# Optimization experiments

Hardware: AMD Instinct MI355X
Metric: run time of the kernel (lower is better)

Reference implementation:

```python
import jax, jax.numpy as jnp
import numpy as np

NUM_GRAPHS = 1024  # static number of segments for global_mean_pool


def setup_inputs() -> dict:
    key = jax.random.key(0)
    ks = jax.random.split(key, 16)
    N, E, F_IN, H = 100000, 1000000, 32, 64
    NUM_ATOM, NUM_ACT, L = 16, 8, 3
    s = 0.05
    x = jax.random.normal(ks[0], (N, F_IN), dtype=jnp.float32)
    edge_index = jax.random.randint(ks[1], (2, E), 0, N, dtype=jnp.int64)
    batch = jnp.sort(jax.random.randint(ks[2], (N,), 0, NUM_GRAPHS, dtype=jnp.int64))
    W_emb = jax.random.normal(ks[3], (F_IN, H), dtype=jnp.float32) * s
    b_emb = jnp.zeros((H,), dtype=jnp.float32)
    W_convs = jax.random.normal(ks[4], (L, H, H), dtype=jnp.float32) * s
    b_convs = jnp.zeros((L, H), dtype=jnp.float32)
    W_act = jax.random.normal(ks[5], (H, NUM_ACT), dtype=jnp.float32) * s
    b_act = jnp.zeros((NUM_ACT,), dtype=jnp.float32)
    W_tgt = jax.random.normal(ks[6], (H, 1), dtype=jnp.float32) * s
    b_tgt = jnp.zeros((1,), dtype=jnp.float32)
    W_atom = jax.random.normal(ks[7], (H, NUM_ATOM), dtype=jnp.float32) * s
    b_atom = jnp.zeros((NUM_ATOM,), dtype=jnp.float32)
    return {"x": x, "edge_index": edge_index, "batch": batch,
            "W_emb": W_emb, "b_emb": b_emb, "W_convs": W_convs, "b_convs": b_convs,
            "W_act": W_act, "b_act": b_act, "W_tgt": W_tgt, "b_tgt": b_tgt,
            "W_atom": W_atom, "b_atom": b_atom}


def reference(x, edge_index, batch, W_emb, b_emb, W_convs, b_convs,
              W_act, b_act, W_tgt, b_tgt, W_atom, b_atom):
    N = x.shape[0]
    # --- GCN normalization with self-loops (PyG GCNConv default) ---
    self_idx = jnp.arange(N, dtype=edge_index.dtype)
    src = jnp.concatenate([edge_index[0], self_idx])  # message source (row)
    dst = jnp.concatenate([edge_index[1], self_idx])  # aggregation target (col)
    ones_e = jnp.ones(src.shape[0], dtype=x.dtype)
    deg = jax.ops.segment_sum(ones_e, dst, num_segments=N)  # in-degree + self-loop
    dinv = jnp.where(deg > 0, jax.lax.rsqrt(deg), 0.0)
    norm = (dinv[src] * dinv[dst])[:, None]  # [E+N, 1]

    h = jax.nn.relu(x @ W_emb + b_emb)  # node embedding
    for i in range(W_convs.shape[0]):
        m = (h @ W_convs[i])[src] * norm            # gather + scale
        agg = jax.ops.segment_sum(m, dst, num_segments=N)  # scatter-add
        h = jax.nn.relu(agg + b_convs[i])

    # --- global mean pool over graphs ---
    cnt = jax.ops.segment_sum(jnp.ones(N, dtype=x.dtype), batch, num_segments=NUM_GRAPHS)
    pooled = jax.ops.segment_sum(h, batch, num_segments=NUM_GRAPHS)
    pooled = pooled / jnp.maximum(cnt, 1.0)[:, None]

    action_type_logits = pooled @ W_act + b_act            # [G, num_action_types]
    target_node_logits = (h @ W_tgt + b_tgt)[:, 0]         # [N]
    new_atom_type_logits = pooled @ W_atom + b_atom        # [G, num_atom_types]
    return (action_type_logits, target_node_logits, new_atom_type_logits, h)
```

## Files before the change

### kernel.cpp

```cpp
#include <hip/hip_runtime.h>
#include <hip/hip_fp16.h>

#define HD 64
#define FIN 32
#define NG 1024
#define STRIDE 64
#define SLOT0 4
#define DEGCAP 59
#define SH 72

#define BINW 128
#define NBMAX 1024
#define EPB 8192
#define BCS 16

typedef _Float16 f16x8 __attribute__((ext_vector_type(8)));
typedef float f32x4 __attribute__((ext_vector_type(4)));
typedef int i32x4 __attribute__((ext_vector_type(4)));

__device__ __forceinline__ int fmap(int jt, int c) {
    return (jt < 2) ? (2 * c + jt) : (32 + 2 * c + (jt - 2));
}

__device__ __forceinline__ void nt_store_h2(__half2 v, __half2* p) {
    __builtin_nontemporal_store(*(int*)&v, (int*)p);
}

__global__ __launch_bounds__(256) void k_zero(int* __restrict__ binCnt, int n) {
    int i = blockIdx.x * 256 + threadIdx.x;
    if (i < n) binCnt[i] = 0;
}

__global__ __launch_bounds__(256) void k_prep(const int* __restrict__ dst,
                                              int* __restrict__ blkBase,
                                              int* __restrict__ binCnt,
                                              int E, int NBINS,
                                              __half2* __restrict__ BaZR,
                                              __half2* __restrict__ BbZR,
                                              const float* __restrict__ Wconv,
                                              __half* __restrict__ Wf, int wtotal,
                                              const float* __restrict__ Wemb,
                                              __half* __restrict__ Wef) {
    __shared__ int hist[NBMAX];
    int b = blockIdx.x, t = threadIdx.x;
    if (b < 48) {
        int tid = b * 256 + t;
        if (tid < wtotal) {
            int layer = tid >> 12;
            int r = tid & 4095;
            int frag = r >> 9, lane = (r >> 3) & 63, e = r & 7;
            int jt = frag >> 1, kh = frag & 1;
            int k = kh * 32 + (lane >> 4) * 8 + e;
            int n = fmap(jt, lane & 15);
            Wf[tid] = (_Float16)Wconv[(size_t)layer * 4096 + k * 64 + n];
        }
    } else if (b < 56) {
        int tid = (b - 48) * 256 + t;
        if (tid < 2048) {
            int jt = tid >> 9, lane = (tid >> 3) & 63, e = tid & 7;
            int k = (lane >> 4) * 8 + e;
            int n = fmap(jt, lane & 15);
            Wef[tid] = (_Float16)Wemb[k * HD + n];
        }
    } else if (b == 56) {
        __half2 z = __floats2half2_rn(0.f, 0.f);
        if (t < 32) BaZR[t] = z;
        else if (t < 64) BbZR[t - 32] = z;
    }
    int e0 = b * EPB;
    if (e0 < E) {
        for (int i = t; i < NBMAX; i += 256) hist[i] = 0;
        __syncthreads();
        int e1 = e0 + EPB; if (e1 > E) e1 = E;
        for (int e = e0 + t; e < e1; e += 256) atomicAdd(&hist[dst[e] >> 7], 1);
        __syncthreads();
        for (int i = t; i < NBINS; i += 256) {
            int h = hist[i];
            if (h) blkBase[b * NBMAX + i] = atomicAdd(&binCnt[i * BCS], h);
        }
    }
}

__global__ __launch_bounds__(1024) void k_scanlite(const int* __restrict__ binCnt,
                                                   int* __restrict__ binStart, int NBINS) {
    __shared__ int s[NBMAX];
    int t = threadIdx.x;
    s[t] = (t < NBINS) ? binCnt[t * BCS] : 0;
    __syncthreads();
    for (int off = 1; off < NBMAX; off <<= 1) {
        int v = s[t];
        int u = (t >= off) ? s[t - off] : 0;
        __syncthreads();
        s[t] = v + u;
        __syncthreads();
    }
    if (t == 0) binStart[0] = 0;
    binStart[t + 1] = s[t];
}

__global__ __launch_bounds__(256) void k_scatter(const int* __restrict__ src,
                                                 const int* __restrict__ dst,
                                                 const int* __restrict__ blkBase,
                                                 const int* __restrict__ binStart,
                                                 int* __restrict__ binned,
                                                 int E, int NBINS) {
    __shared__ int base[NBMAX];
    __shared__ int lpos[NBMAX];
    int b = blockIdx.x, t = threadIdx.x;
    for (int i = t; i < NBMAX; i += 256) {
        lpos[i] = 0;
        base[i] = (i < NBINS) ? (binStart[i] + blkBase[b * NBMAX + i]) : 0;
    }
    __syncthreads();
    int e0 = b * EPB;
    int e1 = e0 + EPB; if (e1 > E) e1 = E;
    for (int e = e0 + t; e < e1; e += 256) {
        int d = dst[e];
        int bin = d >> 7;
        int p = base[bin] + atomicAdd(&lpos[bin], 1);
        binned[p] = (src[e] << 7) | (d & (BINW - 1));
    }
}

__global__ __launch_bounds__(256) void k_csr(const int* __restrict__ binned,
                                             const int* __restrict__ binStart,
                                             int* __restrict__ col, int N) {
    __shared__ int img[BINW * 64];
    __shared__ int cnt[BINW];
    int b = blockIdx.x, t = threadIdx.x;
    for (int i = t; i < BINW * 64; i += 256) img[i] = 0;
    for (int i = t; i < BINW; i += 256) cnt[i] = 0;
    __syncthreads();
    int s = binStart[b], e = binStart[b + 1];
    for (int i = s + t; i < e; i += 256) {
        int w = binned[i];
        int ld = w & (BINW - 1);
        int p = atomicAdd(&cnt[ld], 1);
        if (p < STRIDE - SLOT0) img[ld * 64 + SLOT0 + p] = (int)((unsigned)w >> 7);
    }
    __syncthreads();
    for (int i = t; i < BINW; i += 256) img[i * 64] = cnt[i];
    __syncthreads();
    int v0 = b * BINW;
    int* out = col + ((size_t)v0 << 6);
    for (int j = t; j < BINW * 16; j += 256) {
        int node = v0 + (j >> 4);
        if (node < N) {
            i32x4 val = *(i32x4*)&img[j * 4];
            __builtin_nontemporal_store(val, (i32x4*)(out + j * 4));
        }
    }
}

__device__ __forceinline__ void gemm_from_lds(const __half* hs, const float* dvs,
                                              const float4* __restrict__ Wf4,
                                              __half2* __restrict__ Bout,
                                              int node0, int N, int t) {
    int lane = t & 63;
    int wv = t >> 6;
    int lm = lane & 15, kq = lane >> 4;
    union U { float4 f; f16x8 h; };
    U a0, a1;
    const __half* hrow = hs + (size_t)(wv * 16 + lm) * SH;
    a0.f = *(const float4*)(hrow + kq * 8);
    a1.f = *(const float4*)(hrow + 32 + kq * 8);
    f32x4 acc[4];
#pragma unroll
    for (int jt = 0; jt < 4; jt++) acc[jt] = (f32x4){0.f, 0.f, 0.f, 0.f};
#pragma unroll
    for (int jt = 0; jt < 4; jt++) {
        U b0, b1;
        b0.f = Wf4[(jt * 2 + 0) * 64 + lane];
        b1.f = Wf4[(jt * 2 + 1) * 64 + lane];
        acc[jt] = __builtin_amdgcn_mfma_f32_16x16x32_f16(a0.h, b0.h, acc[jt], 0, 0, 0);
        acc[jt] = __builtin_amdgcn_mfma_f32_16x16x32_f16(a1.h, b1.h, acc[jt], 0, 0, 0);
    }
#pragma unroll
    for (int r = 0; r < 4; r++) {
        int lv = wv * 16 + kq * 4 + r;
        int v = node0 + lv;
        if (v < N) {
            float dv = dvs[lv];
            nt_store_h2(__floats2half2_rn(acc[0][r] * dv, acc[1][r] * dv),
                        Bout + (size_t)v * 32 + lm);
            nt_store_h2(__floats2half2_rn(acc[2][r] * dv, acc[3][r] * dv),
                        Bout + (size_t)v * 32 + 16 + lm);
        }
    }
}

__global__ __launch_bounds__(256) void k_emb_gemm0(const float* __restrict__ x,
                                                   const float4* __restrict__ Wef4,
                                                   const float* __restrict__ bemb,
                                                   const int* __restrict__ col,
                                                   const float4* __restrict__ Wf0,
                                                   __half2* __restrict__ Bout, int N) {
    __shared__ __half hs[64 * SH];
    __shared__ float dvs[64];
    int t = threadIdx.x;
    int lane = t & 63;
    int wv = t >> 6;
    int node0 = blockIdx.x * 64;
    int nodew = node0 + wv * 16;
    int m = lane & 15, kq = lane >> 4;

    int vm = nodew + m;
    if (vm > N - 1) vm = N - 1;
    const float4* xr = (const float4*)(x + (size_t)vm * FIN + kq * 8);
    float4 xa = xr[0], xb = xr[1];
    f16x8 a;
    a[0] = (_Float16)xa.x; a[1] = (_Float16)xa.y; a[2] = (_Float16)xa.z; a[3] = (_Float16)xa.w;
    a[4] = (_Float16)xb.x; a[5] = (_Float16)xb.y; a[6] = (_Float16)xb.z; a[7] = (_Float16)xb.w;

    union U { float4 f; f16x8 h; };
    f32x4 acc[4];
#pragma unroll
    for (int jt = 0; jt < 4; jt++) {
        U b; b.f = Wef4[jt * 64 + lane];
        acc[jt] = (f32x4){0.f, 0.f, 0.f, 0.f};
        acc[jt] = __builtin_amdgcn_mfma_f32_16x16x32_f16(a, b.h, acc[jt], 0, 0, 0);
    }
    float b01x = bemb[2 * m], b01y = bemb[2 * m + 1];
    float b23x = bemb[32 + 2 * m], b23y = bemb[32 + 2 * m + 1];
    __half2 z = __floats2half2_rn(0.f, 0.f);
#pragma unroll
    for (int r = 0; r < 4; r++) {
        int lv = wv * 16 + kq * 4 + r;
        int v = node0 + lv;
        __half2 p01 = z, p23 = z;
        if (v < N) {
            p01 = __floats2half2_rn(fmaxf(acc[0][r] + b01x, 0.f),
                                    fmaxf(acc[1][r] + b01y, 0.f));
            p23 = __floats2half2_rn(fmaxf(acc[2][r] + b23x, 0.f),
                                    fmaxf(acc[3][r] + b23y, 0.f));
        }
        *(__half2*)(hs + (size_t)lv * SH + 2 * m) = p01;
        *(__half2*)(hs + (size_t)lv * SH + 32 + 2 * m) = p23;
        if (m == 0)
            dvs[lv] = (v < N) ? rsqrtf((float)(col[(size_t)v << 6] + 1)) : 1.f;
    }
    __syncthreads();
    gemm_from_lds(hs, dvs, Wf0, Bout, node0, N, t);
}

__global__ __launch_bounds__(256) void k_layer(const __half2* __restrict__ Bin,
                                               const int* __restrict__ col,
                                               const float* __restrict__ bias,
                                               const float4* __restrict__ Wnext,
                                               __half2* __restrict__ Bout,
                                               int N, int ZR) {
    __shared__ __half hs[64 * SH];
    __shared__ float dvs[64];
    int t = threadIdx.x;
    int lane = t & 63;
    int wv = t >> 6;
    int node0 = blockIdx.x * 64;
    int q = lane >> 4, p = lane & 15;
    float4 b4 = *(const float4*)(bias + 4 * p);

#pragma unroll
    for (int pass = 0; pass < 4; pass++) {
        int lv = wv * 16 + pass * 4 + q;
        int v = node0 + lv;
        int vc = (v < N) ? v : 0;
        const int* bucket = col + ((size_t)vc << 6);
        int degraw = bucket[0];
        int deg = degraw > DEGCAP ? DEGCAP : degraw;
        int dmax = deg;
        dmax = max(dmax, __shfl_xor(dmax, 16, 64));
        dmax = max(dmax, __shfl_xor(dmax, 32, 64));
        int rounds = (dmax + 4) >> 2;

        float2 a0 = make_float2(0.f, 0.f), a1 = make_float2(0.f, 0.f);
        for (int rd = 0; rd < rounds; rd++) {
            int4 iq = *(const int4*)(bucket + SLOT0 + rd * 4);
            int idx[4] = {iq.x, iq.y, iq.z, iq.w};
#pragma unroll
            for (int r = 0; r < 4; r++) {
                int i = rd * 4 + r;
                idx[r] = (i < deg) ? idx[r] : ((i == deg) ? vc : ZR);
            }
            float2 raw[4];
#pragma unroll
            for (int r = 0; r < 4; r++)
                raw[r] = *(const float2*)(Bin + (size_t)idx[r] * 32 + p * 2);
#pragma unroll
            for (int r = 0; r < 4; r++) {
                float2 f0 = __half22float2(((const __half2*)&raw[r])[0]);
                float2 f1 = __half22float2(((const __half2*)&raw[r])[1]);
                a0.x += f0.x; a0.y += f0.y; a1.x += f1.x; a1.y += f1.y;
            }
        }
        float dv = rsqrtf((float)(degraw + 1));
        float r0 = fmaxf(dv * a0.x + b4.x, 0.f);
        float r1 = fmaxf(dv * a0.y + b4.y, 0.f);
        float r2 = fmaxf(dv * a1.x + b4.z, 0.f);
        float r3 = fmaxf(dv * a1.y + b4.w, 0.f);
        if (v >= N) { r0 = r1 = r2 = r3 = 0.f; dv = 1.f; }
        __half* hrow = hs + (size_t)lv * SH + 4 * p;
        *(__half2*)(hrow) = __floats2half2_rn(r0, r1);
        *(__half2*)(hrow + 2) = __floats2half2_rn(r2, r3);
        if (p == 0) dvs[lv] = dv;
    }
    __syncthreads();
    gemm_from_lds(hs, dvs, Wnext, Bout, node0, N, t);
}

__global__ __launch_bounds__(256) void k_gather_last(const __half2* __restrict__ Bin,
                                                     const int* __restrict__ col,
                                                     const float* __restrict__ bias,
                                                     float* __restrict__ hout,
                                                     const float* __restrict__ Wtgt,
                                                     const float* __restrict__ btgt,
                                                     float* __restrict__ tgt,
                                                     int N, int ZR) {
    int t = threadIdx.x;
    int lane = t & 63;
    int wv = t >> 6;
    int q = lane >> 4, p = lane & 15;
    int v = blockIdx.x * 16 + wv * 4 + q;
    if (v >= N) return;

    const int* bucket = col + ((size_t)v << 6);
    int degraw = bucket[0];
    int deg = degraw > DEGCAP ? DEGCAP : degraw;
    int dmax = deg;
    dmax = max(dmax, __shfl_xor(dmax, 16, 64));
    dmax = max(dmax, __shfl_xor(dmax, 32, 64));
    int rounds = (dmax + 4) >> 2;

    float2 a0 = make_float2(0.f, 0.f), a1 = make_float2(0.f, 0.f);
    for (int rd = 0; rd < rounds; rd++) {
        int4 iq = *(const int4*)(bucket + SLOT0 + rd * 4);
        int idx[4] = {iq.x, iq.y, iq.z, iq.w};
#pragma unroll
        for (int r = 0; r < 4; r++) {
            int i = rd * 4 + r;
            idx[r] = (i < deg) ? idx[r] : ((i == deg) ? v : ZR);
        }
        float2 raw[4];
#pragma unroll
        for (int r = 0; r < 4; r++)
            raw[r] = *(const float2*)(Bin + (size_t)idx[r] * 32 + p * 2);
#pragma unroll
        for (int r = 0; r < 4; r++) {
            float2 f0 = __half22float2(((const __half2*)&raw[r])[0]);
            float2 f1 = __half22float2(((const __half2*)&raw[r])[1]);
            a0.x += f0.x; a0.y += f0.y; a1.x += f1.x; a1.y += f1.y;
        }
    }
    float dv = rsqrtf((float)(degraw + 1));
    float4 b4 = *(const float4*)(bias + 4 * p);
    float r0 = fmaxf(dv * a0.x + b4.x, 0.f);
    float r1 = fmaxf(dv * a0.y + b4.y, 0.f);
    float r2 = fmaxf(dv * a1.x + b4.z, 0.f);
    float r3 = fmaxf(dv * a1.y + b4.w, 0.f);
    f32x4 o = (f32x4){r0, r1, r2, r3};
    __builtin_nontemporal_store(o, (f32x4*)(hout + (size_t)v * HD + 4 * p));
    float4 w4 = *(const float4*)(Wtgt + 4 * p);
    float pp = r0 * w4.x + r1 * w4.y + r2 * w4.z + r3 * w4.w;
    pp += __shfl_xor(pp, 1, 64); pp += __shfl_xor(pp, 2, 64);
    pp += __shfl_xor(pp, 4, 64); pp += __shfl_xor(pp, 8, 64);
    if (p == 0) __builtin_nontemporal_store(pp + btgt[0], tgt + v);
}

__global__ __launch_bounds__(256) void k_pool(const float* __restrict__ h,
                                              const int* __restrict__ batch,
                                              const float* __restrict__ Wact,
                                              const float* __restrict__ bact,
                                              const float* __restrict__ Watom,
                                              const float* __restrict__ batom,
                                              float* __restrict__ out_act,
                                              float* __restrict__ out_atom, int N) {
    int g = blockIdx.x;
    int t = threadIdx.x;
    int q = t >> 4, p = t & 15;
    int lo = 0, hi = N;
    while (lo < hi) { int mid = (lo + hi) >> 1; if (batch[mid] < g) lo = mid + 1; else hi = mid; }
    int s = lo;
    hi = N;
    while (lo < hi) { int mid = (lo + hi) >> 1; if (batch[mid] < g + 1) lo = mid + 1; else hi = mid; }
    int e2 = lo;
    float4 acc = make_float4(0.f, 0.f, 0.f, 0.f);
    for (int v = s + q; v < e2; v += 16) {
        float4 c = *(const float4*)(h + (size_t)v * HD + p * 4);
        acc.x += c.x; acc.y += c.y; acc.z += c.z; acc.w += c.w;
    }
    __shared__ float4 part[16][16];
    part[q][p] = acc;
    __syncthreads();
    __shared__ float pl[HD];
    if (t < 16) {
        float4 tot = part[0][t];
#pragma unroll
        for (int k = 1; k < 16; k++) {
            float4 c = part[k][t];
            tot.x += c.x; tot.y += c.y; tot.z += c.z; tot.w += c.w;
        }
        float cnt = fmaxf((float)(e2 - s), 1.f);
        pl[t * 4 + 0] = tot.x / cnt; pl[t * 4 + 1] = tot.y / cnt;
        pl[t * 4 + 2] = tot.z / cnt; pl[t * 4 + 3] = tot.w / cnt;
    }
    __syncthreads();
    if (t < 8) {
        float a = bact[t];
#pragma unroll
        for (int k = 0; k < HD; k++) a += pl[k] * Wact[k * 8 + t];
        out_act[g * 8 + t] = a;
    }
    if (t < 16) {
        float a = batom[t];
#pragma unroll
        for (int k = 0; k < HD; k++) a += pl[k] * Watom[k * 16 + t];
        out_atom[g * 16 + t] = a;
    }
}

extern "C" void kernel_launch(void* const* d_in, const int* in_sizes, int n_in,
                              void* d_out, int out_size, void* d_ws, size_t ws_size,
                              hipStream_t stream) {
    const float* x     = (const float*)d_in[0];
    const int*   ei    = (const int*)d_in[1];
    const int*   batch = (const int*)d_in[2];
    const float* Wemb  = (const float*)d_in[3];
    const float* bemb  = (const float*)d_in[4];
    const float* Wconv = (const float*)d_in[5];
    const float* bconv = (const float*)d_in[6];
    const float* Wact  = (const float*)d_in[7];
    const float* bact  = (const float*)d_in[8];
    const float* Wtgt  = (const float*)d_in[9];
    const float* btgt  = (const float*)d_in[10];
    const float* Watom = (const float*)d_in[11];
    const float* batom = (const float*)d_in[12];

    const int N = in_sizes[0] / FIN;
    const int E = in_sizes[1] / 2;
    const int L = in_sizes[5] / (HD * HD);
    const int Npad = (N + 63) & ~63;
    const int ZR = Npad;

    int*     col = (int*)d_ws;
    __half2* Ba  = (__half2*)(col + ((size_t)N << 6));
    __half2* Bb  = Ba + (size_t)(Npad + 64) * 32;
    __half*  Wf  = (__half*)(Bb + (size_t)(Npad + 64) * 32);
    __half*  Wef = Wf + (size_t)L * 4096;

    int* binned   = (int*)Bb;
    int* blkBase  = (int*)((char*)Bb + (8u << 20));
    int* binCnt   = (int*)((char*)Bb + (9u << 20));
    int* binStart = (int*)((char*)Bb + (9u << 20) + (256u << 10));

    const int* srcA = ei;
    const int* dstA = ei + E;

    float* out_act  = (float*)d_out;
    float* out_tgt  = out_act + (size_t)NG * 8;
    float* out_atom = out_tgt + N;
    float* out_h    = out_atom + (size_t)NG * 16;

    const int nbG = (N + 63) / 64;
    const int nbLast = (N + 15) / 16;
    const int wtotal = L * 4096;
    const int nbF1 = (E + EPB - 1) / EPB;
    const int NBINS = (N + BINW - 1) / BINW;
    const int nbPrep = nbF1 > 57 ? nbF1 : 57;
    const int nZero = NBMAX * BCS;

    k_zero<<<(nZero + 255) / 256, 256, 0, stream>>>(binCnt, nZero);
    k_prep<<<nbPrep, 256, 0, stream>>>(dstA, blkBase, binCnt, E, NBINS,
                                       Ba + (size_t)ZR * 32, Bb + (size_t)ZR * 32,
                                       Wconv, Wf, wtotal, Wemb, Wef);
    k_scanlite<<<1, 1024, 0, stream>>>(binCnt, binStart, NBINS);
    k_scatter<<<nbF1, 256, 0, stream>>>(srcA, dstA, blkBase, binStart, binned, E, NBINS);
    k_csr<<<NBINS, 256, 0, stream>>>(binned, binStart, col, N);
    k_emb_gemm0<<<nbG, 256, 0, stream>>>(x, (const float4*)Wef, bemb, col,
                                         (const float4*)Wf, Ba, N);

    __half2* cur = Ba;
    __half2* nxt = Bb;
    for (int l = 0; l < L - 1; ++l) {
        k_layer<<<nbG, 256, 0, stream>>>(cur, col, bconv + l * HD,
                                         (const float4*)(Wf + (size_t)(l + 1) * 4096),
                                         nxt, N, ZR);
        __half2* tmp = cur; cur = nxt; nxt = tmp;
    }
    k_gather_last<<<nbLast, 256, 0, stream>>>(cur, col, bconv + (size_t)(L - 1) * HD,
                                              out_h, Wtgt, btgt, out_tgt, N, ZR);
    k_pool<<<NG, 256, 0, stream>>>(out_h, batch, Wact, bact, Watom, batom,
                                   out_act, out_atom, N);
}
```

Baseline: 242.0 us.

## Replace atomic bin counting with per-bin block-histogram scan and sparse CSR stores

Block histograms are written out directly instead of being reserved with global atomics. A new per-bin kernel column-scans them to produce per-block offsets and bin totals, which removes the zeroing kernel and the single-block scan. Edges are placed into fixed-capacity bins (BINCAP slots per bin), so no global prefix of bin starts is needed. The CSR builder no longer zeroes its LDS image and writes only the 16-byte chunks covering each node's actual degree, cutting global write traffic. The risk is that edges are silently dropped if any bin holds more than BINCAP entries.

After: 238.2 us. Within noise of the previous version (-1.6%).

```diff
diff --git a/kernel.cpp b/kernel.cpp
--- a/kernel.cpp
+++ b/kernel.cpp
@@ -12,7 +12,7 @@
 #define BINW 128
 #define NBMAX 1024
 #define EPB 8192
-#define BCS 16
+#define BINCAP 2048
 
 typedef _Float16 f16x8 __attribute__((ext_vector_type(8)));
 typedef float f32x4 __attribute__((ext_vector_type(4)));
@@ -26,14 +26,8 @@
     __builtin_nontemporal_store(*(int*)&v, (int*)p);
 }
 
-__global__ __launch_bounds__(256) void k_zero(int* __restrict__ binCnt, int n) {
-    int i = blockIdx.x * 256 + threadIdx.x;
-    if (i < n) binCnt[i] = 0;
-}
-
 __global__ __launch_bounds__(256) void k_prep(const int* __restrict__ dst,
-                                              int* __restrict__ blkBase,
-                                              int* __restrict__ binCnt,
+                                              int* __restrict__ blkHist,
                                               int E, int NBINS,
                                               __half2* __restrict__ BaZR,
                                               __half2* __restrict__ BbZR,
@@ -74,34 +68,32 @@
         int e1 = e0 + EPB; if (e1 > E) e1 = E;
         for (int e = e0 + t; e < e1; e += 256) atomicAdd(&hist[dst[e] >> 7], 1);
         __syncthreads();
-        for (int i = t; i < NBINS; i += 256) {
-            int h = hist[i];
-            if (h) blkBase[b * NBMAX + i] = atomicAdd(&binCnt[i * BCS], h);
-        }
-    }
-}
-
-__global__ __launch_bounds__(1024) void k_scanlite(const int* __restrict__ binCnt,
-                                                   int* __restrict__ binStart, int NBINS) {
-    __shared__ int s[NBMAX];
+        for (int i = t; i < NBINS; i += 256) blkHist[b * NBMAX + i] = hist[i];
+    }
+}
+
+__global__ __launch_bounds__(256) void k_scanA(int* __restrict__ blkHist,
+                                               int* __restrict__ binTot, int nb) {
+    __shared__ int s[256];
+    int i = blockIdx.x;
     int t = threadIdx.x;
-    s[t] = (t < NBINS) ? binCnt[t * BCS] : 0;
-    __syncthreads();
-    for (int off = 1; off < NBMAX; off <<= 1) {
+    int x = (t < nb) ? blkHist[t * NBMAX + i] : 0;
+    s[t] = x;
+    __syncthreads();
+    for (int off = 1; off < 256; off <<= 1) {
         int v = s[t];
         int u = (t >= off) ? s[t - off] : 0;
         __syncthreads();
         s[t] = v + u;
         __syncthreads();
     }
-    if (t == 0) binStart[0] = 0;
-    binStart[t + 1] = s[t];
+    if (t < nb) blkHist[t * NBMAX + i] = s[t] - x;
+    if (t == 255) binTot[i] = s[255];
 }
 
 __global__ __launch_bounds__(256) void k_scatter(const int* __restrict__ src,
                                                  const int* __restrict__ dst,
                                                  const int* __restrict__ blkBase,
-                                                 const int* __restrict__ binStart,
                                                  int* __restrict__ binned,
                                                  int E, int NBINS) {
     __shared__ int base[NBMAX];
@@ -109,7 +101,7 @@
     int b = blockIdx.x, t = threadIdx.x;
     for (int i = t; i < NBMAX; i += 256) {
         lpos[i] = 0;
-        base[i] = (i < NBINS) ? (binStart[i] + blkBase[b * NBMAX + i]) : 0;
+        base[i] = (i < NBINS) ? blkBase[b * NBMAX + i] : 0;
     }
     __syncthreads();
     int e0 = b * EPB;
@@ -117,21 +109,23 @@
     for (int e = e0 + t; e < e1; e += 256) {
         int d = dst[e];
         int bin = d >> 7;
-        int p = base[bin] + atomicAdd(&lpos[bin], 1);
-        binned[p] = (src[e] << 7) | (d & (BINW - 1));
+        int off = base[bin] + atomicAdd(&lpos[bin], 1);
+        if (off < BINCAP)
+            binned[bin * BINCAP + off] = (src[e] << 7) | (d & (BINW - 1));
     }
 }
 
 __global__ __launch_bounds__(256) void k_csr(const int* __restrict__ binned,
-                                             const int* __restrict__ binStart,
+                                             const int* __restrict__ binTot,
                                              int* __restrict__ col, int N) {
     __shared__ int img[BINW * 64];
     __shared__ int cnt[BINW];
     int b = blockIdx.x, t = threadIdx.x;
-    for (int i = t; i < BINW * 64; i += 256) img[i] = 0;
     for (int i = t; i < BINW; i += 256) cnt[i] = 0;
     __syncthreads();
-    int s = binStart[b], e = binStart[b + 1];
+    int s = b * BINCAP;
+    int tot = binTot[b]; if (tot > BINCAP) tot = BINCAP;
+    int e = s + tot;
     for (int i = s + t; i < e; i += 256) {
         int w = binned[i];
         int ld = w & (BINW - 1);
@@ -144,8 +138,11 @@
     int v0 = b * BINW;
     int* out = col + ((size_t)v0 << 6);
     for (int j = t; j < BINW * 16; j += 256) {
-        int node = v0 + (j >> 4);
-        if (node < N) {
+        int row = j >> 4, j16 = j & 15;
+        int node = v0 + row;
+        int deg = cnt[row]; if (deg > DEGCAP) deg = DEGCAP;
+        bool keep = (j16 == 0) || (j16 <= ((deg + 3) >> 2));
+        if (node < N && keep) {
             i32x4 val = *(i32x4*)&img[j * 4];
             __builtin_nontemporal_store(val, (i32x4*)(out + j * 4));
         }
@@ -445,10 +442,9 @@
     __half*  Wf  = (__half*)(Bb + (size_t)(Npad + 64) * 32);
     __half*  Wef = Wf + (size_t)L * 4096;
 
-    int* binned   = (int*)Bb;
-    int* blkBase  = (int*)((char*)Bb + (8u << 20));
-    int* binCnt   = (int*)((char*)Bb + (9u << 20));
-    int* binStart = (int*)((char*)Bb + (9u << 20) + (256u << 10));
+    int* binned  = (int*)Bb;
+    int* blkHist = (int*)((char*)Bb + (8u << 20));
+    int* binTot  = (int*)((char*)Bb + (9u << 20));
 
     const int* srcA = ei;
     const int* dstA = ei + E;
@@ -464,15 +460,13 @@
     const int nbF1 = (E + EPB - 1) / EPB;
     const int NBINS = (N + BINW - 1) / BINW;
     const int nbPrep = nbF1 > 57 ? nbF1 : 57;
-    const int nZero = NBMAX * BCS;
-
-    k_zero<<<(nZero + 255) / 256, 256, 0, stream>>>(binCnt, nZero);
-    k_prep<<<nbPrep, 256, 0, stream>>>(dstA, blkBase, binCnt, E, NBINS,
+
+    k_prep<<<nbPrep, 256, 0, stream>>>(dstA, blkHist, E, NBINS,
                                        Ba + (size_t)ZR * 32, Bb + (size_t)ZR * 32,
                                        Wconv, Wf, wtotal, Wemb, Wef);
-    k_scanlite<<<1, 1024, 0, stream>>>(binCnt, binStart, NBINS);
-    k_scatter<<<nbF1, 256, 0, stream>>>(srcA, dstA, blkBase, binStart, binned, E, NBINS);
-    k_csr<<<NBINS, 256, 0, stream>>>(binned, binStart, col, N);
+    k_scanA<<<NBINS, 256, 0, stream>>>(blkHist, binTot, nbF1);
+    k_scatter<<<nbF1, 256, 0, stream>>>(srcA, dstA, blkHist, binned, E, NBINS);
+    k_csr<<<NBINS, 256, 0, stream>>>(binned, binTot, col, N);
     k_emb_gemm0<<<nbG, 256, 0, stream>>>(x, (const float4*)Wef, bemb, col,
                                          (const float4*)Wf, Ba, N);
 
```
